# Optimization experiments

Measured on AMD Instinct MI355X. Metric: run time of the kernel, lower is better.

Reference implementation:

```python
import jax, jax.numpy as jnp
import numpy as np
import math

IN_DIM = 3
N_LEVELS = 16
F = 2
LOG2_T = 19
T = 2 ** LOG2_T
BASE_RES = 16
FINEST_RES = 512
N_POINTS = 1048576

# Per-level resolutions (static, matches torch buffer construction)
_b = math.exp((math.log(FINEST_RES) - math.log(BASE_RES)) / max(N_LEVELS - 1, 1))
RES = np.array([int(BASE_RES * _b ** i) for i in range(N_LEVELS)], dtype=np.int32)  # [L]
# XOR spatial-hash primes (dim 0 uses prime 1)
PRIMES = np.array([1, 2654435761, 805459861, 3674653429], dtype=np.uint32)


def _hash(coords_u32):
    """coords_u32: (..., IN_DIM) uint32 -> int32 hash in [0, T).
    uint32 wraparound arithmetic gives the same low-19 bits as torch's int64
    math, since T divides 2**32 and XOR/product low bits are self-contained."""
    h = coords_u32[..., 0]
    for d in range(1, IN_DIM):
        h = h ^ (coords_u32[..., d] * PRIMES[d % len(PRIMES)])
    return (h & jnp.uint32(T - 1)).astype(jnp.int32)


def setup_inputs() -> dict:
    key = jax.random.key(0)
    k1, k2 = jax.random.split(key)
    x = jax.random.uniform(k1, (N_POINTS, IN_DIM), dtype=jnp.float32)  # coords in [0,1]
    embeddings = jax.random.uniform(
        k2, (N_LEVELS, T, F), minval=-1e-4, maxval=1e-4, dtype=jnp.float32
    )
    return {"x": x, "embeddings": embeddings}


def reference(x, embeddings):
    N = x.shape[0]
    res_f = jnp.asarray(RES, dtype=x.dtype)            # [L]
    res_i = jnp.asarray(RES, dtype=jnp.int32)          # [L]

    # Scale all levels at once: [L, N, D]
    x_scaled = x[None, :, :] * (res_f[:, None, None] - 1.0)
    x_floor = jnp.clip(x_scaled.astype(jnp.int32), 0, res_i[:, None, None] - 2)
    x_frac = x_scaled - x_floor.astype(x.dtype)        # [L, N, D]

    feat = jnp.zeros((N_LEVELS, N, F), dtype=x.dtype)
    for corner in range(2 ** IN_DIM):                  # fixed 8 corners
        off = np.array([(corner >> d) & 1 for d in range(IN_DIM)], dtype=np.int32)
        corner_coords = jnp.clip(x_floor + off, 0, res_i[:, None, None] - 1)
        h = _hash(corner_coords.astype(jnp.uint32))    # [L, N]
        # gather per-level features: embeddings[l, h[l, n]] -> [L, N, F]
        corner_feat = jnp.take_along_axis(embeddings, h[:, :, None], axis=1)
        # N-linear weight: prod over dims of frac or (1-frac)
        w = jnp.prod(
            jnp.where(off.astype(bool), x_frac, 1.0 - x_frac),
            axis=-1, keepdims=True,
        )                                              # [L, N, 1]
        feat = feat + w * corner_feat

    # concat levels along feature dim: [N, L*F]
    return jnp.moveaxis(feat, 0, 1).reshape(N, N_LEVELS * F)
```

## Files before the change

### kernel.cpp

```cpp
#include <hip/hip_runtime.h>
#include <math.h>
#include <stdint.h>

#define LOG2_T 19
#define T_SIZE (1u << LOG2_T)
#define T_MASK (T_SIZE - 1u)
#define N_LEVELS 16
#define N_CELL 5
#define N_HASH 11
#define PRIME1 2654435761u
#define PRIME2 805459861u

typedef unsigned long long u64;
typedef float f4v __attribute__((ext_vector_type(4)));

struct Params {
    int res[N_LEVELS];
    int dOff[N_CELL];
    int cellOffC[N_CELL + 1];
    int cellTot;
};

__device__ __forceinline__ float bf_lo(uint32_t v) { return __uint_as_float(v << 16); }
__device__ __forceinline__ float bf_hi(uint32_t v) { return __uint_as_float(v & 0xFFFF0000u); }

__device__ __forceinline__ uint32_t f32_to_bf16_rne(float f) {
    uint32_t u = __float_as_uint(f);
    u += 0x7FFFu + ((u >> 16) & 1u);
    return u >> 16;
}
__device__ __forceinline__ uint32_t pack2(float2 e) {
    return f32_to_bf16_rne(e.x) | (f32_to_bf16_rne(e.y) << 16);
}

__device__ __forceinline__ float2 nt_load_f2(const float2* p) {
    union { float2 f; u64 u; } cv;
    cv.u = __builtin_nontemporal_load((const u64*)p);
    return cv.f;
}
__device__ __forceinline__ void nt_store_f2(float2 v, float2* p) {
    union { float2 f; u64 u; } cv; cv.f = v;
    __builtin_nontemporal_store(cv.u, (u64*)p);
}

__device__ __forceinline__ uint32_t sel4(uint4 q, uint32_t s) {
    const uint32_t a = (s & 1u) ? q.y : q.x;
    const uint32_t b = (s & 1u) ? q.w : q.z;
    return (s & 2u) ? b : a;
}

__global__ __launch_bounds__(256) void hg_build_fine(
    const float2* __restrict__ emb, uint32_t* __restrict__ tabF)
{
    const int i = blockIdx.x * 256 + threadIdx.x;
    tabF[i] = pack2(emb[(size_t)N_CELL * T_SIZE + i]);
}

__global__ __launch_bounds__(256) void hg_build_cell(
    const float2* __restrict__ emb, uint32_t* __restrict__ tabD, Params P)
{
    const int i = blockIdx.x * 256 + threadIdx.x;
    if (i >= P.cellTot * 8) return;
    const int cg = i >> 3, k = i & 7;
    int l = 0;
    while (l < N_CELL - 1 && cg >= P.cellOffC[l + 1]) ++l;
    const int e = cg - P.cellOffC[l];
    const int C = P.res[l] - 1;
    const int ix = e % C; const int r = e / C; const int iy = r % C; const int iz = r / C;
    const uint32_t xx = (uint32_t)(ix + (k & 1));
    const uint32_t yy = (uint32_t)(iy + ((k >> 1) & 1));
    const uint32_t zz = (uint32_t)(iz + (k >> 2));
    const uint32_t h = (xx ^ (yy * PRIME1) ^ (zz * PRIME2)) & T_MASK;
    tabD[P.dOff[l] + e * 8 + k] = pack2(emb[(size_t)l * T_SIZE + h]);
}

struct Pt { int ix, iy, iz; float fx, fy, fz; };

__device__ __forceinline__ Pt mk_pt(float x0, float x1, float x2,
                                    int rl, float rf) {
    Pt p;
    const float sx = x0 * rf, sy = x1 * rf, sz = x2 * rf;
    int ix = (int)sx; ix = ix < 0 ? 0 : (ix > rl - 2 ? rl - 2 : ix);
    int iy = (int)sy; iy = iy < 0 ? 0 : (iy > rl - 2 ? rl - 2 : iy);
    int iz = (int)sz; iz = iz < 0 ? 0 : (iz > rl - 2 ? rl - 2 : iz);
    p.ix = ix; p.iy = iy; p.iz = iz;
    p.fx = sx - (float)ix; p.fy = sy - (float)iy; p.fz = sz - (float)iz;
    return p;
}

__device__ __forceinline__ float2 blend8s(
    uint32_t c0, uint32_t c1, uint32_t c2, uint32_t c3,
    uint32_t c4, uint32_t c5, uint32_t c6, uint32_t c7,
    float fx, float fy, float fz)
{
    const float wx0 = 1.0f - fx, wx1 = fx;
    const float wy0 = 1.0f - fy, wy1 = fy;
    const float wz0 = 1.0f - fz, wz1 = fz;
    float w, f0 = 0.0f, f1 = 0.0f;
    w = wx0 * wy0 * wz0; f0 = fmaf(w, bf_lo(c0), f0); f1 = fmaf(w, bf_hi(c0), f1);
    w = wx1 * wy0 * wz0; f0 = fmaf(w, bf_lo(c1), f0); f1 = fmaf(w, bf_hi(c1), f1);
    w = wx0 * wy1 * wz0; f0 = fmaf(w, bf_lo(c2), f0); f1 = fmaf(w, bf_hi(c2), f1);
    w = wx1 * wy1 * wz0; f0 = fmaf(w, bf_lo(c3), f0); f1 = fmaf(w, bf_hi(c3), f1);
    w = wx0 * wy0 * wz1; f0 = fmaf(w, bf_lo(c4), f0); f1 = fmaf(w, bf_hi(c4), f1);
    w = wx1 * wy0 * wz1; f0 = fmaf(w, bf_lo(c5), f0); f1 = fmaf(w, bf_hi(c5), f1);
    w = wx0 * wy1 * wz1; f0 = fmaf(w, bf_lo(c6), f0); f1 = fmaf(w, bf_hi(c6), f1);
    w = wx1 * wy1 * wz1; f0 = fmaf(w, bf_lo(c7), f0); f1 = fmaf(w, bf_hi(c7), f1);
    float2 o; o.x = f0; o.y = f1;
    return o;
}

__global__ __launch_bounds__(256, 6) void hg_levels(
    const float* __restrict__ x,
    const uint32_t* __restrict__ tabF,
    const uint32_t* __restrict__ tabD,
    float2* __restrict__ feat,
    int N, Params P)
{
    const int l = blockIdx.x & 15;
    const int n = (blockIdx.x >> 4) * 256 + threadIdx.x;
    if (n >= N) return;

    const int rl = P.res[l];
    const float rf = (float)(rl - 1);
    const Pt p = mk_pt(x[n * 3 + 0], x[n * 3 + 1], x[n * 3 + 2], rl, rf);

    float2 o;
    if (l < N_CELL) {
        const uint32_t* __restrict__ t = tabD + P.dOff[l];
        const int C = rl - 1;
        const uint32_t* cb = t + (size_t)((p.iz * C + p.iy) * C + p.ix) * 8;
        const uint4 q0 = *(const uint4*)cb;
        const uint4 q1 = *(const uint4*)(cb + 4);
        __builtin_amdgcn_sched_barrier(0);
        o = blend8s(q0.x, q0.y, q0.z, q0.w, q1.x, q1.y, q1.z, q1.w,
                    p.fx, p.fy, p.fz);
    } else {
        const uint32_t* __restrict__ t = tabF + (size_t)(l - N_CELL) * T_SIZE;
        const uint32_t hx = (uint32_t)p.ix;
        const uint32_t dx = hx ^ (hx + 1u);
        const uint32_t y0 = (uint32_t)p.iy * PRIME1, y1 = y0 + PRIME1;
        const uint32_t z0 = (uint32_t)p.iz * PRIME2, z1 = z0 + PRIME2;
        const uint32_t i00 = (hx ^ y0 ^ z0) & T_MASK;
        const uint32_t i10 = (hx ^ y1 ^ z0) & T_MASK;
        const uint32_t i01 = (hx ^ y0 ^ z1) & T_MASK;
        const uint32_t i11 = (hx ^ y1 ^ z1) & T_MASK;
        const uint4 q00 = *(const uint4*)(t + (i00 & ~3u));
        const uint4 q10 = *(const uint4*)(t + (i10 & ~3u));
        const uint4 q01 = *(const uint4*)(t + (i01 & ~3u));
        const uint4 q11 = *(const uint4*)(t + (i11 & ~3u));
        uint32_t s1 = 0, s3 = 0, s5 = 0, s7 = 0;
        const bool in4 = (dx < 4u);
        if (!in4) {
            s1 = t[(i00 ^ dx) & T_MASK];
            s3 = t[(i10 ^ dx) & T_MASK];
            s5 = t[(i01 ^ dx) & T_MASK];
            s7 = t[(i11 ^ dx) & T_MASK];
        }
        __builtin_amdgcn_sched_barrier(0);
        const uint32_t c0 = sel4(q00, i00 & 3u);
        const uint32_t c2 = sel4(q10, i10 & 3u);
        const uint32_t c4 = sel4(q01, i01 & 3u);
        const uint32_t c6 = sel4(q11, i11 & 3u);
        const uint32_t c1 = in4 ? sel4(q00, (i00 ^ dx) & 3u) : s1;
        const uint32_t c3 = in4 ? sel4(q10, (i10 ^ dx) & 3u) : s3;
        const uint32_t c5 = in4 ? sel4(q01, (i01 ^ dx) & 3u) : s5;
        const uint32_t c7 = in4 ? sel4(q11, (i11 ^ dx) & 3u) : s7;
        o = blend8s(c0, c1, c2, c3, c4, c5, c6, c7, p.fx, p.fy, p.fz);
    }

    nt_store_f2(o, &feat[(size_t)l * N + n]);
}

__global__ __launch_bounds__(256) void hg_transpose(
    const float2* __restrict__ feat, f4v* __restrict__ out, int N)
{
    __shared__ float2 st[N_LEVELS][131];
    const int base = blockIdx.x * 128;
    const int t = threadIdx.x;
#pragma unroll
    for (int i = 0; i < 4; ++i) {
        const int idx = i * 256 + t;
        const int l = idx >> 6, pp = (idx & 63) * 2;
        const int n = base + pp;
        float2 v0 = make_float2(0.f, 0.f), v1 = v0;
        if (n + 1 < N) {
            const f4v q = __builtin_nontemporal_load((const f4v*)&feat[(size_t)l * N + n]);
            v0.x = q.x; v0.y = q.y; v1.x = q.z; v1.y = q.w;
        } else if (n < N) {
            v0 = nt_load_f2(&feat[(size_t)l * N + n]);
        }
        st[l][pp] = v0; st[l][pp + 1] = v1;
    }
    __syncthreads();
#pragma unroll
    for (int i = 0; i < 4; ++i) {
        const int idx = i * 256 + t;
        const int p = idx >> 3, k = idx & 7;
        const int n = base + p;
        if (n < N) {
            const float2 a = st[2 * k][p], b = st[2 * k + 1][p];
            f4v o; o.x = a.x; o.y = a.y; o.z = b.x; o.w = b.y;
            __builtin_nontemporal_store(o, &out[(size_t)n * 8 + k]);
        }
    }
}

__global__ __launch_bounds__(256) void hg_fallback(
    const float* __restrict__ x, const float* __restrict__ emb,
    float* __restrict__ out, int N, Params P)
{
    const int gid = blockIdx.x * 256 + threadIdx.x;
    const int n = gid >> 4, l = gid & 15;
    if (n >= N) return;
    const int rl = P.res[l];
    const float rf = (float)(rl - 1);
    float sx = x[n * 3 + 0] * rf, sy = x[n * 3 + 1] * rf, sz = x[n * 3 + 2] * rf;
    int ix = (int)sx; ix = ix < 0 ? 0 : (ix > rl - 2 ? rl - 2 : ix);
    int iy = (int)sy; iy = iy < 0 ? 0 : (iy > rl - 2 ? rl - 2 : iy);
    int iz = (int)sz; iz = iz < 0 ? 0 : (iz > rl - 2 ? rl - 2 : iz);
    const float fx = sx - ix, fy = sy - iy, fz = sz - iz;
    const uint32_t hx0 = (uint32_t)ix, hx1 = hx0 + 1u;
    const uint32_t hy0 = (uint32_t)iy * PRIME1, hy1 = hy0 + PRIME1;
    const uint32_t hz0 = (uint32_t)iz * PRIME2, hz1 = hz0 + PRIME2;
    const float2* tab = (const float2*)emb + (size_t)l * T_SIZE;
    float2 e0 = tab[(hx0 ^ hy0 ^ hz0) & T_MASK], e1 = tab[(hx1 ^ hy0 ^ hz0) & T_MASK];
    float2 e2 = tab[(hx0 ^ hy1 ^ hz0) & T_MASK], e3 = tab[(hx1 ^ hy1 ^ hz0) & T_MASK];
    float2 e4 = tab[(hx0 ^ hy0 ^ hz1) & T_MASK], e5 = tab[(hx1 ^ hy0 ^ hz1) & T_MASK];
    float2 e6 = tab[(hx0 ^ hy1 ^ hz1) & T_MASK], e7 = tab[(hx1 ^ hy1 ^ hz1) & T_MASK];
    const float wx0 = 1.0f - fx, wx1 = fx, wy0 = 1.0f - fy, wy1 = fy, wz0 = 1.0f - fz, wz1 = fz;
    float w, f0 = 0.0f, f1 = 0.0f;
    w = wx0 * wy0 * wz0; f0 = fmaf(w, e0.x, f0); f1 = fmaf(w, e0.y, f1);
    w = wx1 * wy0 * wz0; f0 = fmaf(w, e1.x, f0); f1 = fmaf(w, e1.y, f1);
    w = wx0 * wy1 * wz0; f0 = fmaf(w, e2.x, f0); f1 = fmaf(w, e2.y, f1);
    w = wx1 * wy1 * wz0; f0 = fmaf(w, e3.x, f0); f1 = fmaf(w, e3.y, f1);
    w = wx0 * wy0 * wz1; f0 = fmaf(w, e4.x, f0); f1 = fmaf(w, e4.y, f1);
    w = wx1 * wy0 * wz1; f0 = fmaf(w, e5.x, f0); f1 = fmaf(w, e5.y, f1);
    w = wx0 * wy1 * wz1; f0 = fmaf(w, e6.x, f0); f1 = fmaf(w, e6.y, f1);
    w = wx1 * wy1 * wz1; f0 = fmaf(w, e7.x, f0); f1 = fmaf(w, e7.y, f1);
    float2 o; o.x = f0; o.y = f1;
    ((float2*)out)[(size_t)n * N_LEVELS + l] = o;
}

extern "C" void kernel_launch(void* const* d_in, const int* in_sizes, int n_in,
                              void* d_out, int out_size, void* d_ws, size_t ws_size,
                              hipStream_t stream) {
    const float* x   = (const float*)d_in[0];
    const float* emb = (const float*)d_in[1];
    const int N = in_sizes[0] / 3;

    Params P;
    const double b = exp((log(512.0) - log(16.0)) / 15.0);
    for (int i = 0; i < N_LEVELS; ++i)
        P.res[i] = (int)(16.0 * pow(b, (double)i));

    P.cellOffC[0] = 0;
    for (int l = 0; l < N_CELL; ++l) {
        const int C = P.res[l] - 1;
        P.cellOffC[l + 1] = P.cellOffC[l] + C * C * C;
    }
    P.cellTot = P.cellOffC[N_CELL];
    for (int l = 0; l < N_CELL; ++l) P.dOff[l] = P.cellOffC[l] * 8;

    const size_t fine_bytes  = (size_t)N_HASH * T_SIZE * sizeof(uint32_t);
    const size_t dense_bytes = ((size_t)P.cellTot * 8 * sizeof(uint32_t) + 255) & ~255ull;
    const size_t feat_bytes  = (size_t)N_LEVELS * N * sizeof(float2);

    if (ws_size >= fine_bytes + dense_bytes + feat_bytes) {
        uint32_t* tabF = (uint32_t*)d_ws;
        uint32_t* tabD = (uint32_t*)((char*)d_ws + fine_bytes);
        float2*   feat = (float2*)((char*)d_ws + fine_bytes + dense_bytes);

        hipLaunchKernelGGL(hg_build_fine, dim3(N_HASH * T_SIZE / 256), dim3(256), 0, stream,
                           (const float2*)emb, tabF);
        hipLaunchKernelGGL(hg_build_cell, dim3((P.cellTot * 8 + 255) / 256), dim3(256), 0, stream,
                           (const float2*)emb, tabD, P);

        const int chunks = (N + 255) / 256;
        hipLaunchKernelGGL(hg_levels, dim3(chunks * 16), dim3(256), 0, stream,
                           x, tabF, tabD, feat, N, P);

        hipLaunchKernelGGL(hg_transpose, dim3((N + 127) / 128), dim3(256), 0, stream,
                           feat, (f4v*)d_out, N);
    } else {
        hipLaunchKernelGGL(hg_fallback, dim3((N * 16 + 255) / 256), dim3(256), 0, stream,
                           x, emb, (float*)d_out, N, P);
    }
}
```

Baseline: 542.4 us.

## Map hash levels to XCDs for L2 locality and drop nontemporal transpose accesses

Reassigns blocks in the levels kernel so each XCD (blockIdx mod 8) works on one or two fixed levels, keeping each level's hash table resident in that XCD's L2. The three XCDs that own the heaviest levels (8-10) also take a share of levels 13-15 to balance work, and surplus blocks exit early. It also switches the transpose kernel's feat loads and output stores from nontemporal to normal accesses. The cost is idle blocks from the oversized grid and a dependence on round-robin block-to-XCD dispatch.

```diff
diff --git a/kernel.cpp b/kernel.cpp
--- a/kernel.cpp
+++ b/kernel.cpp
@@ -19,6 +19,8 @@
     int dOff[N_CELL];
     int cellOffC[N_CELL + 1];
     int cellTot;
+    int chunks;
+    int don;
 };
 
 __device__ __forceinline__ float bf_lo(uint32_t v) { return __uint_as_float(v << 16); }
@@ -33,11 +35,6 @@
     return f32_to_bf16_rne(e.x) | (f32_to_bf16_rne(e.y) << 16);
 }
 
-__device__ __forceinline__ float2 nt_load_f2(const float2* p) {
-    union { float2 f; u64 u; } cv;
-    cv.u = __builtin_nontemporal_load((const u64*)p);
-    return cv.f;
-}
 __device__ __forceinline__ void nt_store_f2(float2 v, float2* p) {
     union { float2 f; u64 u; } cv; cv.f = v;
     __builtin_nontemporal_store(cv.u, (u64*)p);
@@ -116,8 +113,22 @@
     float2* __restrict__ feat,
     int N, Params P)
 {
-    const int l = blockIdx.x & 15;
-    const int n = (blockIdx.x >> 4) * 256 + threadIdx.x;
+    const int xcd = blockIdx.x & 7;
+    const int w   = blockIdx.x >> 3;
+    const int ch  = P.chunks, D = P.don;
+
+    int l, chunk;
+    if (w < ch) { l = xcd; chunk = w; }
+    else if (xcd < 3) {
+        if (w < 2 * ch) { l = xcd + 8; chunk = w - ch; }
+        else            { l = 13 + xcd; chunk = (ch - D) + (w - 2 * ch); }
+    } else if (xcd < 5) {
+        if (w < 2 * ch) { l = xcd + 8; chunk = w - ch; } else return;
+    } else {
+        if (w < 2 * ch - D) { l = xcd + 8; chunk = w - ch; } else return;
+    }
+
+    const int n = chunk * 256 + threadIdx.x;
     if (n >= N) return;
 
     const int rl = P.res[l];
@@ -184,10 +195,10 @@
         const int n = base + pp;
         float2 v0 = make_float2(0.f, 0.f), v1 = v0;
         if (n + 1 < N) {
-            const f4v q = __builtin_nontemporal_load((const f4v*)&feat[(size_t)l * N + n]);
+            const f4v q = *(const f4v*)&feat[(size_t)l * N + n];
             v0.x = q.x; v0.y = q.y; v1.x = q.z; v1.y = q.w;
         } else if (n < N) {
-            v0 = nt_load_f2(&feat[(size_t)l * N + n]);
+            v0 = feat[(size_t)l * N + n];
         }
         st[l][pp] = v0; st[l][pp + 1] = v1;
     }
@@ -200,7 +211,7 @@
         if (n < N) {
             const float2 a = st[2 * k][p], b = st[2 * k + 1][p];
             f4v o; o.x = a.x; o.y = a.y; o.z = b.x; o.w = b.y;
-            __builtin_nontemporal_store(o, &out[(size_t)n * 8 + k]);
+            out[(size_t)n * 8 + k] = o;
         }
     }
 }
@@ -261,6 +272,9 @@
     P.cellTot = P.cellOffC[N_CELL];
     for (int l = 0; l < N_CELL; ++l) P.dOff[l] = P.cellOffC[l] * 8;
 
+    P.chunks = (N + 255) / 256;
+    P.don    = (P.chunks * 3) / 10;
+
     const size_t fine_bytes  = (size_t)N_HASH * T_SIZE * sizeof(uint32_t);
     const size_t dense_bytes = ((size_t)P.cellTot * 8 * sizeof(uint32_t) + 255) & ~255ull;
     const size_t feat_bytes  = (size_t)N_LEVELS * N * sizeof(float2);
@@ -275,8 +289,7 @@
         hipLaunchKernelGGL(hg_build_cell, dim3((P.cellTot * 8 + 255) / 256), dim3(256), 0, stream,
                            (const float2*)emb, tabD, P);
 
-        const int chunks = (N + 255) / 256;
-        hipLaunchKernelGGL(hg_levels, dim3(chunks * 16), dim3(256), 0, stream,
+        hipLaunchKernelGGL(hg_levels, dim3(8 * (2 * P.chunks + P.don)), dim3(256), 0, stream,
                            x, tabF, tabD, feat, N, P);
 
         hipLaunchKernelGGL(hg_transpose, dim3((N + 127) / 128), dim3(256), 0, stream,
```

Measured after the change: 509.2 us. 6.1% less time.
